# Performance work log

Hardware: AMD Instinct MI355X
Metric: run time of the kernel (lower is better)

## Reference

```python
import jax, jax.numpy as jnp
import numpy as np

N = 50000
E = 800000
IN_DIM = 128
OUT_DIM = 128


def setup_inputs() -> dict:
    key = jax.random.key(0)
    k1, k2, k3, k4, k5, k6 = jax.random.split(key, 6)
    x = jax.random.normal(k1, (N, IN_DIM), dtype=jnp.float32)
    edge_index = jax.random.randint(k2, (2, E), 0, N, dtype=jnp.int64)
    # Linear params (PyTorch default init: U(-1/sqrt(fan_in), 1/sqrt(fan_in)))
    bound = 1.0 / np.sqrt(IN_DIM)
    w_self = jax.random.uniform(k3, (OUT_DIM, IN_DIM), minval=-bound, maxval=bound, dtype=jnp.float32)
    b_self = jax.random.uniform(k4, (OUT_DIM,), minval=-bound, maxval=bound, dtype=jnp.float32)
    w_neigh = jax.random.uniform(k5, (OUT_DIM, IN_DIM), minval=-bound, maxval=bound, dtype=jnp.float32)
    b_neigh = jax.random.uniform(k6, (OUT_DIM,), minval=-bound, maxval=bound, dtype=jnp.float32)
    return {"x": x, "edge_index": edge_index, "w_self": w_self, "b_self": b_self,
            "w_neigh": w_neigh, "b_neigh": b_neigh}


def reference(x, edge_index, w_self, b_self, w_neigh, b_neigh):
    src = edge_index[0]
    dst = edge_index[1]
    n = x.shape[0]
    # scatter-add neighbor features: agg[dst] += x[src]
    agg = jax.ops.segment_sum(x[src], dst, num_segments=n)  # [N, in_dim]
    # in-degree count, clamped at 1
    deg = jax.ops.segment_sum(jnp.ones((src.shape[0],), dtype=x.dtype), dst, num_segments=n)
    deg = jnp.maximum(deg, 1.0)[:, None]  # [N, 1]
    mean_neigh = agg / deg
    return x @ w_self.T + b_self + mean_neigh @ w_neigh.T + b_neigh
```

## Files before the change

kernel.cpp:

```cpp
#include <hip/hip_runtime.h>

#define DIM 128
#define NT 256
#define BUCK 32
#define PCH 4096
#define NBMAX 2048
#define BAT 256
#define CAPB 1024
#define CONV_BLKS 512
#define WPACK_BLKS 16

typedef __attribute__((ext_vector_type(8))) short short8;
typedef __attribute__((ext_vector_type(8))) unsigned short ushort8;
typedef __attribute__((ext_vector_type(4))) float f32x4;
typedef __attribute__((ext_vector_type(2))) float f32x2;

static __device__ __forceinline__ unsigned short f32_to_bf16(float f) {
    union { float f; unsigned int u; } c; c.f = f;
    unsigned int u = c.u;
    u += 0x7FFFu + ((u >> 16) & 1u);
    return (unsigned short)(u >> 16);
}

__global__ void setup_partition_kernel(const float* __restrict__ x, const int* __restrict__ ei,
                                       const float* __restrict__ w_self, const float* __restrict__ b_self,
                                       const float* __restrict__ w_neigh, const float* __restrict__ b_neigh,
                                       unsigned short* __restrict__ xb, unsigned int* __restrict__ xf8,
                                       unsigned short* __restrict__ w_swz,
                                       float* __restrict__ bias, int* __restrict__ gcur,
                                       int* __restrict__ ovfc, unsigned int* __restrict__ csr,
                                       unsigned int* __restrict__ ovf,
                                       int n4, int E, int NB, int PBLKS) {
    int b = blockIdx.x, t = threadIdx.x;
    if (b < PBLKS) {
        __shared__ int hist[NBMAX];
        __shared__ int base[NBMAX];
        __shared__ int avail[NBMAX];
        __shared__ int obase[NBMAX];
        __shared__ int lcur[NBMAX];
        int cbase = b * PCH;
        int cend = min(E, cbase + PCH);
        for (int i = t; i < NB; i += NT) { hist[i] = 0; lcur[i] = 0; }
        __syncthreads();
        for (int e = cbase + t; e < cend; e += NT)
            atomicAdd(&hist[ei[E + e] >> 5], 1);
        __syncthreads();
        for (int bk = t; bk < NB; bk += NT) {
            int c = hist[bk];
            if (c) {
                int r = atomicAdd(&gcur[bk], c);
                int av = (r < CAPB) ? min(c, CAPB - r) : 0;
                base[bk] = r;
                avail[bk] = av;
                obase[bk] = (c > av) ? atomicAdd(ovfc, c - av) : 0;
            }
        }
        __syncthreads();
        for (int e = cbase + t; e < cend; e += NT) {
            unsigned int src = (unsigned int)ei[e];
            unsigned int dst = (unsigned int)ei[E + e];
            int bk = (int)(dst >> 5);
            int idx = atomicAdd(&lcur[bk], 1);
            unsigned int pk = (dst << 16) | src;
            if (idx < avail[bk]) csr[(size_t)bk * CAPB + base[bk] + idx] = pk;
            else ovf[obase[bk] + idx - avail[bk]] = pk;
        }
    } else if (b < PBLKS + CONV_BLKS) {
        for (int g = (b - PBLKS) * NT + t; g < n4; g += CONV_BLKS * NT) {
            float4 v = reinterpret_cast<const float4*>(x)[g];
            ushort4 s = make_ushort4(f32_to_bf16(v.x), f32_to_bf16(v.y),
                                     f32_to_bf16(v.z), f32_to_bf16(v.w));
            reinterpret_cast<ushort4*>(xb)[g] = s;
            int p = __builtin_amdgcn_cvt_pk_fp8_f32(v.x, v.y, 0, false);
            p = __builtin_amdgcn_cvt_pk_fp8_f32(v.z, v.w, p, true);
            xf8[g] = (unsigned int)p;
        }
    } else {
        int g = (b - PBLKS - CONV_BLKS) * NT + t;
        if (g < 128) bias[g] = b_self[g] + b_neigh[g];
        if (g >= 64 * 64) return;
        int f = g >> 6, l = g & 63;
        int ks = f >> 3, nf = f & 7;
        int j = nf * 16 + (l & 15);
        int kbase = ks * 32 + ((l >> 4) << 3);
#pragma unroll
        for (int e = 0; e < 8; ++e) {
            int k = kbase + e;
            float v = (k < 128) ? w_self[(size_t)j * 128 + k]
                                : w_neigh[(size_t)j * 128 + (k - 128)];
            w_swz[((size_t)g << 3) + e] = f32_to_bf16(v);
        }
    }
}

__global__ void __launch_bounds__(BAT)
fused_aggregate_kernel(const unsigned short* __restrict__ xb,
                       const unsigned int* __restrict__ xf8,
                       const int* __restrict__ gcur,
                       const int* __restrict__ ovfc,
                       const unsigned int* __restrict__ csr,
                       const unsigned int* __restrict__ ovf,
                       const unsigned short* __restrict__ w_swz,
                       const float* __restrict__ bias,
                       float* __restrict__ out, int n) {
    __shared__ unsigned short srt[CAPB];
    __shared__ unsigned short xm[BUCK][264];
    __shared__ int bin[BUCK];
    __shared__ int boff_s[BUCK + 1];
    __shared__ int cur[BUCK];

    int tid = threadIdx.x, wid = tid >> 6, lane = tid & 63;
    int grp = lane >> 4, j = lane & 15;
    int b0 = blockIdx.x;
    int bsize = min(gcur[b0], CAPB);
    int ovfn = ovfc[0];
    const unsigned int* my = csr + (size_t)b0 * CAPB;
    int gbase = b0 * BUCK;
    const uint2* x8 = reinterpret_cast<const uint2*>(xf8);

    for (int fi = tid; fi < BUCK * 16; fi += BAT) {
        int row = fi >> 4, c = fi & 15;
        int grow = gbase + row;
        ushort8 s = (ushort8)0;
        if (grow < n) s = reinterpret_cast<const ushort8*>(xb + (size_t)grow * DIM)[c];
        *reinterpret_cast<ushort8*>(&xm[row][c * 8]) = s;
    }

    for (int i = tid; i < BUCK; i += BAT) bin[i] = 0;
    __syncthreads();
    for (int i = tid; i < bsize; i += BAT)
        atomicAdd(&bin[(my[i] >> 16) & 31], 1);
    __syncthreads();
    if (wid == 0) {
        int v = (lane < BUCK) ? bin[lane] : 0;
        int s = v;
        for (int d = 1; d < BUCK; d <<= 1) {
            int u = __shfl_up(s, d, 64);
            if (lane >= d) s += u;
        }
        if (lane < BUCK) {
            boff_s[lane] = s - v;
            cur[lane] = s - v;
            if (lane == BUCK - 1) boff_s[BUCK] = s;
        }
    }
    __syncthreads();
    for (int i = tid; i < bsize; i += BAT) {
        unsigned int p = my[i];
        int d = (p >> 16) & 31;
        srt[atomicAdd(&cur[d], 1)] = (unsigned short)(p & 0xFFFFu);
    }
    __syncthreads();

#pragma unroll 2
    for (int i = 0; i < 8; ++i) {
        int nd = wid * 8 + i;
        int s = boff_s[nd], epd = boff_s[nd + 1];
        float acc[8];
#pragma unroll
        for (int k = 0; k < 8; ++k) acc[k] = 0.f;
        for (int e = s; e < epd; e += 16) {
            uint2 v[4];
#pragma unroll
            for (int q = 0; q < 4; ++q) {
                int eidx = e + q * 4 + grp;
                bool ok = eidx < epd;
                int src = srt[ok ? eidx : s];
                uint2 tv = x8[(size_t)src * 16 + j];
                if (!ok) tv = make_uint2(0u, 0u);
                v[q] = tv;
            }
#pragma unroll
            for (int q = 0; q < 4; ++q) {
                f32x2 a0 = __builtin_amdgcn_cvt_pk_f32_fp8(v[q].x, false);
                f32x2 a1 = __builtin_amdgcn_cvt_pk_f32_fp8(v[q].x, true);
                f32x2 b0 = __builtin_amdgcn_cvt_pk_f32_fp8(v[q].y, false);
                f32x2 b1 = __builtin_amdgcn_cvt_pk_f32_fp8(v[q].y, true);
                acc[0] += a0.x; acc[1] += a0.y; acc[2] += a1.x; acc[3] += a1.y;
                acc[4] += b0.x; acc[5] += b0.y; acc[6] += b1.x; acc[7] += b1.y;
            }
        }
        int deg = epd - s;
        for (int o = 0; o < ovfn; ++o) {
            unsigned int p = ovf[o];
            if ((int)(p >> 16) == gbase + nd) {
                uint2 tv = x8[(size_t)(p & 0xFFFFu) * 16 + j];
                f32x2 a0 = __builtin_amdgcn_cvt_pk_f32_fp8(tv.x, false);
                f32x2 a1 = __builtin_amdgcn_cvt_pk_f32_fp8(tv.x, true);
                f32x2 b0 = __builtin_amdgcn_cvt_pk_f32_fp8(tv.y, false);
                f32x2 b1 = __builtin_amdgcn_cvt_pk_f32_fp8(tv.y, true);
                acc[0] += a0.x; acc[1] += a0.y; acc[2] += a1.x; acc[3] += a1.y;
                acc[4] += b0.x; acc[5] += b0.y; acc[6] += b1.x; acc[7] += b1.y;
                ++deg;
            }
        }
#pragma unroll
        for (int k = 0; k < 8; ++k) {
            acc[k] += __shfl_xor(acc[k], 16);
            acc[k] += __shfl_xor(acc[k], 32);
        }
        float inv = deg > 0 ? 1.0f / (float)deg : 0.f;
        if (grp == 0) {
            ushort8 m = (ushort8)0;
#pragma unroll
            for (int k = 0; k < 8; ++k) m[k] = f32_to_bf16(acc[k] * inv);
            *reinterpret_cast<ushort8*>(&xm[nd][128 + j * 8]) = m;
        }
    }
    __syncthreads();

    int rg = wid >> 1, ch = wid & 1;
    int arow = rg * 16 + (lane & 15);
    int koff = (lane >> 4) << 3;

    f32x4 acc[4];
#pragma unroll
    for (int nf = 0; nf < 4; ++nf) acc[nf] = (f32x4){0.f, 0.f, 0.f, 0.f};

#pragma unroll
    for (int ks = 0; ks < 8; ++ks) {
        short8 a = *reinterpret_cast<const short8*>(&xm[arow][ks * 32 + koff]);
#pragma unroll
        for (int nf = 0; nf < 4; ++nf) {
            int f = ks * 8 + ch * 4 + nf;
            short8 b = *reinterpret_cast<const short8*>(w_swz + (((size_t)f * 64 + lane) << 3));
            acc[nf] = __builtin_amdgcn_mfma_f32_16x16x32_bf16(a, b, acc[nf], 0, 0, 0);
        }
    }

    int crow0 = rg * 16 + ((lane >> 4) << 2);
#pragma unroll
    for (int nf = 0; nf < 4; ++nf) {
        int col = (ch * 4 + nf) * 16 + (lane & 15);
        float bs = bias[col];
#pragma unroll
        for (int r = 0; r < 4; ++r) {
            int grow = gbase + crow0 + r;
            if (grow < n) out[(size_t)grow * DIM + col] = acc[nf][r] + bs;
        }
    }
}

extern "C" void kernel_launch(void* const* d_in, const int* in_sizes, int n_in,
                              void* d_out, int out_size, void* d_ws, size_t ws_size,
                              hipStream_t stream) {
    const float* x       = (const float*)d_in[0];
    const int*   ei      = (const int*)d_in[1];
    const float* w_self  = (const float*)d_in[2];
    const float* b_self  = (const float*)d_in[3];
    const float* w_neigh = (const float*)d_in[4];
    const float* b_neigh = (const float*)d_in[5];
    float* out = (float*)d_out;

    int n = in_sizes[0] / DIM;
    int E = in_sizes[1] / 2;
    int NB = (n + BUCK - 1) / BUCK;

    int* gcur = (int*)d_ws;
    int* ovfc = gcur + NBMAX;
    unsigned int* csr = (unsigned int*)(ovfc + 4);
    unsigned int* ovf = csr + (size_t)NB * CAPB;
    unsigned short* w_swz = (unsigned short*)(((uintptr_t)(ovf + E) + 15) & ~(uintptr_t)15);
    float* bias = (float*)(w_swz + 64 * 64 * 8);
    unsigned short* x_bf = (unsigned short*)(bias + 128);
    unsigned int* x_fp8 = (unsigned int*)(x_bf + (size_t)n * DIM);

    hipMemsetAsync(gcur, 0, (NBMAX + 4) * sizeof(int), stream);

    int n4 = n * DIM / 4;
    int PBLKS = (E + PCH - 1) / PCH;
    setup_partition_kernel<<<PBLKS + CONV_BLKS + WPACK_BLKS, NT, 0, stream>>>(
        x, ei, w_self, b_self, w_neigh, b_neigh, x_bf, x_fp8, w_swz, bias,
        gcur, ovfc, csr, ovf, n4, E, NB, PBLKS);

    fused_aggregate_kernel<<<NB, BAT, 0, stream>>>(x_bf, x_fp8, gcur, ovfc, csr, ovf,
                                                   w_swz, bias, out, n);
}
```

Measured before the change: 72.99 us.

## Interleave gathers for two destination nodes per wave and enlarge partition chunk

The aggregation loop now processes two destination nodes at once, issuing eight independent fp8 row gathers per iteration instead of four. This raises memory-level parallelism and hides gather latency. Accumulation uses packed f32x2 adds, and a fast path for empty buckets skips the histogram and sort steps. PCH is also doubled, which changes the partition chunk size. The cost is higher register pressure and wasted iterations when the two nodes' degrees differ.

Result: slower. 96.73 us (+32.5%).

```diff
diff --git a/kernel.cpp b/kernel.cpp
--- a/kernel.cpp
+++ b/kernel.cpp
@@ -3,7 +3,7 @@
 #define DIM 128
 #define NT 256
 #define BUCK 32
-#define PCH 4096
+#define PCH 8192
 #define NBMAX 2048
 #define BAT 256
 #define CAPB 1024
@@ -126,85 +126,110 @@
         *reinterpret_cast<ushort8*>(&xm[row][c * 8]) = s;
     }
 
-    for (int i = tid; i < BUCK; i += BAT) bin[i] = 0;
-    __syncthreads();
-    for (int i = tid; i < bsize; i += BAT)
-        atomicAdd(&bin[(my[i] >> 16) & 31], 1);
-    __syncthreads();
-    if (wid == 0) {
-        int v = (lane < BUCK) ? bin[lane] : 0;
-        int s = v;
-        for (int d = 1; d < BUCK; d <<= 1) {
-            int u = __shfl_up(s, d, 64);
-            if (lane >= d) s += u;
-        }
-        if (lane < BUCK) {
-            boff_s[lane] = s - v;
-            cur[lane] = s - v;
-            if (lane == BUCK - 1) boff_s[BUCK] = s;
-        }
-    }
-    __syncthreads();
-    for (int i = tid; i < bsize; i += BAT) {
-        unsigned int p = my[i];
-        int d = (p >> 16) & 31;
-        srt[atomicAdd(&cur[d], 1)] = (unsigned short)(p & 0xFFFFu);
-    }
-    __syncthreads();
-
-#pragma unroll 2
-    for (int i = 0; i < 8; ++i) {
-        int nd = wid * 8 + i;
-        int s = boff_s[nd], epd = boff_s[nd + 1];
-        float acc[8];
-#pragma unroll
-        for (int k = 0; k < 8; ++k) acc[k] = 0.f;
-        for (int e = s; e < epd; e += 16) {
-            uint2 v[4];
-#pragma unroll
-            for (int q = 0; q < 4; ++q) {
-                int eidx = e + q * 4 + grp;
-                bool ok = eidx < epd;
-                int src = srt[ok ? eidx : s];
-                uint2 tv = x8[(size_t)src * 16 + j];
-                if (!ok) tv = make_uint2(0u, 0u);
-                v[q] = tv;
-            }
-#pragma unroll
-            for (int q = 0; q < 4; ++q) {
-                f32x2 a0 = __builtin_amdgcn_cvt_pk_f32_fp8(v[q].x, false);
-                f32x2 a1 = __builtin_amdgcn_cvt_pk_f32_fp8(v[q].x, true);
-                f32x2 b0 = __builtin_amdgcn_cvt_pk_f32_fp8(v[q].y, false);
-                f32x2 b1 = __builtin_amdgcn_cvt_pk_f32_fp8(v[q].y, true);
-                acc[0] += a0.x; acc[1] += a0.y; acc[2] += a1.x; acc[3] += a1.y;
-                acc[4] += b0.x; acc[5] += b0.y; acc[6] += b1.x; acc[7] += b1.y;
-            }
-        }
-        int deg = epd - s;
-        for (int o = 0; o < ovfn; ++o) {
-            unsigned int p = ovf[o];
-            if ((int)(p >> 16) == gbase + nd) {
-                uint2 tv = x8[(size_t)(p & 0xFFFFu) * 16 + j];
-                f32x2 a0 = __builtin_amdgcn_cvt_pk_f32_fp8(tv.x, false);
-                f32x2 a1 = __builtin_amdgcn_cvt_pk_f32_fp8(tv.x, true);
-                f32x2 b0 = __builtin_amdgcn_cvt_pk_f32_fp8(tv.y, false);
-                f32x2 b1 = __builtin_amdgcn_cvt_pk_f32_fp8(tv.y, true);
-                acc[0] += a0.x; acc[1] += a0.y; acc[2] += a1.x; acc[3] += a1.y;
-                acc[4] += b0.x; acc[5] += b0.y; acc[6] += b1.x; acc[7] += b1.y;
-                ++deg;
-            }
-        }
-#pragma unroll
-        for (int k = 0; k < 8; ++k) {
-            acc[k] += __shfl_xor(acc[k], 16);
-            acc[k] += __shfl_xor(acc[k], 32);
-        }
-        float inv = deg > 0 ? 1.0f / (float)deg : 0.f;
+    if (bsize > 0) {
+        for (int i = tid; i < BUCK; i += BAT) bin[i] = 0;
+        __syncthreads();
+        for (int i = tid; i < bsize; i += BAT)
+            atomicAdd(&bin[(my[i] >> 16) & 31], 1);
+        __syncthreads();
+        if (wid == 0) {
+            int v = (lane < BUCK) ? bin[lane] : 0;
+            int s = v;
+            for (int d = 1; d < BUCK; d <<= 1) {
+                int u = __shfl_up(s, d, 64);
+                if (lane >= d) s += u;
+            }
+            if (lane < BUCK) {
+                boff_s[lane] = s - v;
+                cur[lane] = s - v;
+                if (lane == BUCK - 1) boff_s[BUCK] = s;
+            }
+        }
+        __syncthreads();
+        for (int i = tid; i < bsize; i += BAT) {
+            unsigned int p = my[i];
+            int d = (p >> 16) & 31;
+            srt[atomicAdd(&cur[d], 1)] = (unsigned short)(p & 0xFFFFu);
+        }
+        __syncthreads();
+
+#pragma unroll
+        for (int ii = 0; ii < 8; ii += 2) {
+            int nd0 = wid * 8 + ii, nd1 = nd0 + 1;
+            int s0 = boff_s[nd0], end0 = boff_s[nd0 + 1];
+            int s1 = boff_s[nd1], end1 = boff_s[nd1 + 1];
+            f32x2 ac0[4], ac1[4];
+#pragma unroll
+            for (int k = 0; k < 4; ++k) { ac0[k] = (f32x2){0.f, 0.f}; ac1[k] = (f32x2){0.f, 0.f}; }
+            int iters = max((end0 - s0 + 15) >> 4, (end1 - s1 + 15) >> 4);
+            int e0 = s0, e1 = s1;
+            for (int it = 0; it < iters; ++it, e0 += 16, e1 += 16) {
+                uint2 v0[4], v1[4];
+#pragma unroll
+                for (int q = 0; q < 4; ++q) {
+                    int i0 = e0 + q * 4 + grp;
+                    bool ok0 = i0 < end0;
+                    uint2 t0 = x8[(size_t)srt[ok0 ? i0 : s0] * 16 + j];
+                    v0[q] = ok0 ? t0 : make_uint2(0u, 0u);
+                    int i1 = e1 + q * 4 + grp;
+                    bool ok1 = i1 < end1;
+                    uint2 t1 = x8[(size_t)srt[ok1 ? i1 : s1] * 16 + j];
+                    v1[q] = ok1 ? t1 : make_uint2(0u, 0u);
+                }
+#pragma unroll
+                for (int q = 0; q < 4; ++q) {
+                    ac0[0] += __builtin_amdgcn_cvt_pk_f32_fp8(v0[q].x, false);
+                    ac0[1] += __builtin_amdgcn_cvt_pk_f32_fp8(v0[q].x, true);
+                    ac0[2] += __builtin_amdgcn_cvt_pk_f32_fp8(v0[q].y, false);
+                    ac0[3] += __builtin_amdgcn_cvt_pk_f32_fp8(v0[q].y, true);
+                    ac1[0] += __builtin_amdgcn_cvt_pk_f32_fp8(v1[q].x, false);
+                    ac1[1] += __builtin_amdgcn_cvt_pk_f32_fp8(v1[q].x, true);
+                    ac1[2] += __builtin_amdgcn_cvt_pk_f32_fp8(v1[q].y, false);
+                    ac1[3] += __builtin_amdgcn_cvt_pk_f32_fp8(v1[q].y, true);
+                }
+            }
+            int dg0 = end0 - s0, dg1 = end1 - s1;
+            for (int o = 0; o < ovfn; ++o) {
+                unsigned int p = ovf[o];
+                int pd = (int)(p >> 16);
+                if (pd == gbase + nd0 || pd == gbase + nd1) {
+                    uint2 tv = x8[(size_t)(p & 0xFFFFu) * 16 + j];
+                    f32x2* ac = (pd == gbase + nd0) ? ac0 : ac1;
+                    ac[0] += __builtin_amdgcn_cvt_pk_f32_fp8(tv.x, false);
+                    ac[1] += __builtin_amdgcn_cvt_pk_f32_fp8(tv.x, true);
+                    ac[2] += __builtin_amdgcn_cvt_pk_f32_fp8(tv.y, false);
+                    ac[3] += __builtin_amdgcn_cvt_pk_f32_fp8(tv.y, true);
+                    if (pd == gbase + nd0) ++dg0; else ++dg1;
+                }
+            }
+#pragma unroll
+            for (int half = 0; half < 2; ++half) {
+                f32x2* ac = half ? ac1 : ac0;
+                int nd = half ? nd1 : nd0;
+                int deg = half ? dg1 : dg0;
+                float t[8];
+#pragma unroll
+                for (int k = 0; k < 4; ++k) { t[2 * k] = ac[k].x; t[2 * k + 1] = ac[k].y; }
+#pragma unroll
+                for (int k = 0; k < 8; ++k) {
+                    t[k] += __shfl_xor(t[k], 16);
+                    t[k] += __shfl_xor(t[k], 32);
+                }
+                float inv = deg > 0 ? 1.0f / (float)deg : 0.f;
+                if (grp == 0) {
+                    ushort8 m = (ushort8)0;
+#pragma unroll
+                    for (int k = 0; k < 8; ++k) m[k] = f32_to_bf16(t[k] * inv);
+                    *reinterpret_cast<ushort8*>(&xm[nd][128 + j * 8]) = m;
+                }
+            }
+        }
+    } else {
         if (grp == 0) {
-            ushort8 m = (ushort8)0;
-#pragma unroll
-            for (int k = 0; k < 8; ++k) m[k] = f32_to_bf16(acc[k] * inv);
-            *reinterpret_cast<ushort8*>(&xm[nd][128 + j * 8]) = m;
+            ushort8 z = (ushort8)0;
+#pragma unroll
+            for (int i = 0; i < 8; ++i)
+                *reinterpret_cast<ushort8*>(&xm[wid * 8 + i][128 + j * 8]) = z;
         }
     }
     __syncthreads();
```

## Halve node bucket size, enlarge partition chunks, and slim partition shared state

Applied to the files above, without the earlier changes.

Buckets now hold 16 destination nodes instead of 32. The aggregate kernel runs 128 threads per block, and each wave computes one column half of a single 16-row MFMA tile. The partition phase uses 512-thread blocks over 8192-edge chunks. Shared state is packed into one base/avail word, the histogram array is reused as the local cursor, and overflow slots are claimed with a per-edge global atomic. The accumulators are rewritten as packed float2 adds. The aim is more aggregate blocks for better parallelism and less LDS in the partition kernel, at the cost of more global atomics on gcur and possible per-edge overflow contention.

Result: faster. 66.24 us (-9.2%).

```diff
diff --git a/kernel.cpp b/kernel.cpp
--- a/kernel.cpp
+++ b/kernel.cpp
@@ -1,14 +1,14 @@
 #include <hip/hip_runtime.h>
 
 #define DIM 128
-#define NT 256
-#define BUCK 32
-#define PCH 4096
-#define NBMAX 2048
-#define BAT 256
-#define CAPB 1024
-#define CONV_BLKS 512
-#define WPACK_BLKS 16
+#define BUCK 16
+#define PCH 8192
+#define NBMAX 4096
+#define BAT 128
+#define CAPB 512
+#define NTS 512
+#define CONV_BLKS 256
+#define WPACK_BLKS 8
 
 typedef __attribute__((ext_vector_type(8))) short short8;
 typedef __attribute__((ext_vector_type(8))) unsigned short ushort8;
@@ -22,51 +22,53 @@
     return (unsigned short)(u >> 16);
 }
 
-__global__ void setup_partition_kernel(const float* __restrict__ x, const int* __restrict__ ei,
-                                       const float* __restrict__ w_self, const float* __restrict__ b_self,
-                                       const float* __restrict__ w_neigh, const float* __restrict__ b_neigh,
-                                       unsigned short* __restrict__ xb, unsigned int* __restrict__ xf8,
-                                       unsigned short* __restrict__ w_swz,
-                                       float* __restrict__ bias, int* __restrict__ gcur,
-                                       int* __restrict__ ovfc, unsigned int* __restrict__ csr,
-                                       unsigned int* __restrict__ ovf,
-                                       int n4, int E, int NB, int PBLKS) {
+__global__ void __launch_bounds__(NTS)
+setup_partition_kernel(const float* __restrict__ x, const int* __restrict__ ei,
+                       const float* __restrict__ w_self, const float* __restrict__ b_self,
+                       const float* __restrict__ w_neigh, const float* __restrict__ b_neigh,
+                       unsigned short* __restrict__ xb, unsigned int* __restrict__ xf8,
+                       unsigned short* __restrict__ w_swz,
+                       float* __restrict__ bias, int* __restrict__ gcur,
+                       int* __restrict__ ovfc, unsigned int* __restrict__ csr,
+                       unsigned int* __restrict__ ovf,
+                       int n4, int E, int NB, int PBLKS) {
     int b = blockIdx.x, t = threadIdx.x;
     if (b < PBLKS) {
         __shared__ int hist[NBMAX];
-        __shared__ int base[NBMAX];
-        __shared__ int avail[NBMAX];
-        __shared__ int obase[NBMAX];
-        __shared__ int lcur[NBMAX];
+        __shared__ unsigned int bav[NBMAX];
         int cbase = b * PCH;
         int cend = min(E, cbase + PCH);
-        for (int i = t; i < NB; i += NT) { hist[i] = 0; lcur[i] = 0; }
+        for (int i = t; i < NB; i += NTS) hist[i] = 0;
         __syncthreads();
-        for (int e = cbase + t; e < cend; e += NT)
-            atomicAdd(&hist[ei[E + e] >> 5], 1);
+        for (int e = cbase + t; e < cend; e += NTS)
+            atomicAdd(&hist[ei[E + e] >> 4], 1);
         __syncthreads();
-        for (int bk = t; bk < NB; bk += NT) {
+        for (int bk = t; bk < NB; bk += NTS) {
             int c = hist[bk];
+            unsigned int pack = 0;
             if (c) {
                 int r = atomicAdd(&gcur[bk], c);
-                int av = (r < CAPB) ? min(c, CAPB - r) : 0;
-                base[bk] = r;
-                avail[bk] = av;
-                obase[bk] = (c > av) ? atomicAdd(ovfc, c - av) : 0;
-            }
+                int base = min(r, CAPB);
+                int av = min(c, CAPB - base);
+                pack = ((unsigned int)base << 16) | (unsigned int)av;
+            }
+            bav[bk] = pack;
+            hist[bk] = 0;
         }
         __syncthreads();
-        for (int e = cbase + t; e < cend; e += NT) {
+        for (int e = cbase + t; e < cend; e += NTS) {
             unsigned int src = (unsigned int)ei[e];
             unsigned int dst = (unsigned int)ei[E + e];
-            int bk = (int)(dst >> 5);
-            int idx = atomicAdd(&lcur[bk], 1);
+            int bk = (int)(dst >> 4);
+            int idx = atomicAdd(&hist[bk], 1);
             unsigned int pk = (dst << 16) | src;
-            if (idx < avail[bk]) csr[(size_t)bk * CAPB + base[bk] + idx] = pk;
-            else ovf[obase[bk] + idx - avail[bk]] = pk;
+            unsigned int pa = bav[bk];
+            int base = (int)(pa >> 16), av = (int)(pa & 0xFFFFu);
+            if (idx < av) csr[(size_t)bk * CAPB + base + idx] = pk;
+            else ovf[atomicAdd(ovfc, 1)] = pk;
         }
     } else if (b < PBLKS + CONV_BLKS) {
-        for (int g = (b - PBLKS) * NT + t; g < n4; g += CONV_BLKS * NT) {
+        for (int g = (b - PBLKS) * NTS + t; g < n4; g += CONV_BLKS * NTS) {
             float4 v = reinterpret_cast<const float4*>(x)[g];
             ushort4 s = make_ushort4(f32_to_bf16(v.x), f32_to_bf16(v.y),
                                      f32_to_bf16(v.z), f32_to_bf16(v.w));
@@ -76,7 +78,7 @@
             xf8[g] = (unsigned int)p;
         }
     } else {
-        int g = (b - PBLKS - CONV_BLKS) * NT + t;
+        int g = (b - PBLKS - CONV_BLKS) * NTS + t;
         if (g < 128) bias[g] = b_self[g] + b_neigh[g];
         if (g >= 64 * 64) return;
         int f = g >> 6, l = g & 63;
@@ -129,11 +131,12 @@
     for (int i = tid; i < BUCK; i += BAT) bin[i] = 0;
     __syncthreads();
     for (int i = tid; i < bsize; i += BAT)
-        atomicAdd(&bin[(my[i] >> 16) & 31], 1);
+        atomicAdd(&bin[(my[i] >> 16) & 15], 1);
     __syncthreads();
     if (wid == 0) {
         int v = (lane < BUCK) ? bin[lane] : 0;
         int s = v;
+#pragma unroll
         for (int d = 1; d < BUCK; d <<= 1) {
             int u = __shfl_up(s, d, 64);
             if (lane >= d) s += u;
@@ -147,7 +150,7 @@
     __syncthreads();
     for (int i = tid; i < bsize; i += BAT) {
         unsigned int p = my[i];
-        int d = (p >> 16) & 31;
+        int d = (p >> 16) & 15;
         srt[atomicAdd(&cur[d], 1)] = (unsigned short)(p & 0xFFFFu);
     }
     __syncthreads();
@@ -156,28 +159,22 @@
     for (int i = 0; i < 8; ++i) {
         int nd = wid * 8 + i;
         int s = boff_s[nd], epd = boff_s[nd + 1];
-        float acc[8];
-#pragma unroll
-        for (int k = 0; k < 8; ++k) acc[k] = 0.f;
+        f32x2 c0 = {0.f, 0.f}, c1 = {0.f, 0.f}, c2 = {0.f, 0.f}, c3 = {0.f, 0.f};
         for (int e = s; e < epd; e += 16) {
             uint2 v[4];
 #pragma unroll
             for (int q = 0; q < 4; ++q) {
                 int eidx = e + q * 4 + grp;
                 bool ok = eidx < epd;
-                int src = srt[ok ? eidx : s];
-                uint2 tv = x8[(size_t)src * 16 + j];
-                if (!ok) tv = make_uint2(0u, 0u);
-                v[q] = tv;
+                uint2 tv = x8[(size_t)srt[ok ? eidx : s] * 16 + j];
+                v[q] = ok ? tv : make_uint2(0u, 0u);
             }
 #pragma unroll
             for (int q = 0; q < 4; ++q) {
-                f32x2 a0 = __builtin_amdgcn_cvt_pk_f32_fp8(v[q].x, false);
-                f32x2 a1 = __builtin_amdgcn_cvt_pk_f32_fp8(v[q].x, true);
-                f32x2 b0 = __builtin_amdgcn_cvt_pk_f32_fp8(v[q].y, false);
-                f32x2 b1 = __builtin_amdgcn_cvt_pk_f32_fp8(v[q].y, true);
-                acc[0] += a0.x; acc[1] += a0.y; acc[2] += a1.x; acc[3] += a1.y;
-                acc[4] += b0.x; acc[5] += b0.y; acc[6] += b1.x; acc[7] += b1.y;
+                c0 += __builtin_amdgcn_cvt_pk_f32_fp8(v[q].x, false);
+                c1 += __builtin_amdgcn_cvt_pk_f32_fp8(v[q].x, true);
+                c2 += __builtin_amdgcn_cvt_pk_f32_fp8(v[q].y, false);
+                c3 += __builtin_amdgcn_cvt_pk_f32_fp8(v[q].y, true);
             }
         }
         int deg = epd - s;
@@ -185,32 +182,31 @@
             unsigned int p = ovf[o];
             if ((int)(p >> 16) == gbase + nd) {
                 uint2 tv = x8[(size_t)(p & 0xFFFFu) * 16 + j];
-                f32x2 a0 = __builtin_amdgcn_cvt_pk_f32_fp8(tv.x, false);
-                f32x2 a1 = __builtin_amdgcn_cvt_pk_f32_fp8(tv.x, true);
-                f32x2 b0 = __builtin_amdgcn_cvt_pk_f32_fp8(tv.y, false);
-                f32x2 b1 = __builtin_amdgcn_cvt_pk_f32_fp8(tv.y, true);
-                acc[0] += a0.x; acc[1] += a0.y; acc[2] += a1.x; acc[3] += a1.y;
-                acc[4] += b0.x; acc[5] += b0.y; acc[6] += b1.x; acc[7] += b1.y;
+                c0 += __builtin_amdgcn_cvt_pk_f32_fp8(tv.x, false);
+                c1 += __builtin_amdgcn_cvt_pk_f32_fp8(tv.x, true);
+                c2 += __builtin_amdgcn_cvt_pk_f32_fp8(tv.y, false);
+                c3 += __builtin_amdgcn_cvt_pk_f32_fp8(tv.y, true);
                 ++deg;
             }
         }
+        float t[8] = {c0.x, c0.y, c1.x, c1.y, c2.x, c2.y, c3.x, c3.y};
 #pragma unroll
         for (int k = 0; k < 8; ++k) {
-            acc[k] += __shfl_xor(acc[k], 16);
-            acc[k] += __shfl_xor(acc[k], 32);
+            t[k] += __shfl_xor(t[k], 16);
+            t[k] += __shfl_xor(t[k], 32);
         }
         float inv = deg > 0 ? 1.0f / (float)deg : 0.f;
         if (grp == 0) {
             ushort8 m = (ushort8)0;
 #pragma unroll
-            for (int k = 0; k < 8; ++k) m[k] = f32_to_bf16(acc[k] * inv);
+            for (int k = 0; k < 8; ++k) m[k] = f32_to_bf16(t[k] * inv);
             *reinterpret_cast<ushort8*>(&xm[nd][128 + j * 8]) = m;
         }
     }
     __syncthreads();
 
-    int rg = wid >> 1, ch = wid & 1;
-    int arow = rg * 16 + (lane & 15);
+    int ch = wid;
+    int arow = lane & 15;
     int koff = (lane >> 4) << 3;
 
     f32x4 acc[4];
@@ -228,7 +224,7 @@
         }
     }
 
-    int crow0 = rg * 16 + ((lane >> 4) << 2);
+    int crow0 = (lane >> 4) << 2;
 #pragma unroll
     for (int nf = 0; nf < 4; ++nf) {
         int col = (ch * 4 + nf) * 16 + (lane & 15);
@@ -269,7 +265,7 @@
 
     int n4 = n * DIM / 4;
     int PBLKS = (E + PCH - 1) / PCH;
-    setup_partition_kernel<<<PBLKS + CONV_BLKS + WPACK_BLKS, NT, 0, stream>>>(
+    setup_partition_kernel<<<PBLKS + CONV_BLKS + WPACK_BLKS, NTS, 0, stream>>>(
         x, ei, w_self, b_self, w_neigh, b_neigh, x_bf, x_fp8, w_swz, bias,
         gcur, ovfc, csr, ovf, n4, E, NB, PBLKS);
 
```
